# Kernel optimization log

Hardware: AMD Instinct MI355X
Metric: run time of the kernel (lower is better)

Reference implementation:

```python
import jax, jax.numpy as jnp
import numpy as np

B, H, W_DIM, C = 16, 128, 128, 256

def setup_inputs() -> dict:
    key = jax.random.key(0)
    k1, k2, k3 = jax.random.split(key, 3)
    grid = jax.random.normal(k1, (B, H, W_DIM, C), dtype=jnp.float32)
    # nn.Linear(2C, C): weight [C, 2C], bias [C]; store transposed for x @ W
    W = jax.random.normal(k2, (2 * C, C), dtype=jnp.float32) * (1.0 / np.sqrt(2 * C))
    b = jax.random.normal(k3, (C,), dtype=jnp.float32) * 0.01
    return {"grid": grid, "W": W, "b": b}

def reference(grid, W, b):
    # cumulative max along width (axis=2) and height (axis=1)
    x_cummax = jax.lax.cummax(grid, axis=2)
    y_cummax = jax.lax.cummax(grid, axis=1)
    result = jnp.concatenate([x_cummax, y_cummax], axis=-1)  # [B,H,W,2C]
    return result @ W + b  # [B,H,W,C]
```

## Files before the change

### kernel.cpp

```cpp
#include <hip/hip_runtime.h>
#include <hip/hip_fp16.h>

#define BB 16
#define HH 128
#define WW 128
#define CC 256

typedef __attribute__((ext_vector_type(8))) short s16x8;
typedef __attribute__((ext_vector_type(8))) unsigned short u16x8;
typedef __attribute__((ext_vector_type(4))) float f32x4;
typedef __attribute__((ext_vector_type(4))) int i32x4;

__device__ static inline unsigned short f2bf(float x) {
    union { float f; unsigned u; } v; v.f = x;
    unsigned r = v.u + 0x7fffu + ((v.u >> 16) & 1u);
    return (unsigned short)(r >> 16);
}
__device__ static inline float bf2f(unsigned short u) {
    union { unsigned u; float f; } v; v.u = (unsigned)u << 16; return v.f;
}
__device__ static inline unsigned short h2u(__half h) {
    unsigned short u; __builtin_memcpy(&u, &h, 2); return u;
}
__device__ static inline float u2f16(unsigned short u) {
    __half h; __builtin_memcpy(&h, &u, 2); return __half2float(h);
}
__device__ static inline int sidx(int row, int col) {
    return row * 256 + (((col >> 3) ^ (row & 7)) << 3) + (col & 7);
}
__device__ static inline int sidx4(int row, int c4) {
    return row * 256 + (((c4 >> 1) ^ (row & 7)) << 3) + (c4 & 1) * 4;
}

__global__ __launch_bounds__(256) void conv_w_kernel(const float* __restrict__ Wf,
                                                     unsigned short* __restrict__ Wt) {
    const int i = blockIdx.x * 256 + threadIdx.x;
    const int n = i & 255, k = i >> 8;
    const int hy = k >> 8, g = (k >> 3) & 31, j = k & 7;
    Wt[hy * 65536 + ((size_t)(g * 256 + n) << 3) + j] = f2bf(Wf[i]);
}

template <bool NT>
__device__ __forceinline__ void scan16_to_lds(const f32x4* __restrict__ base, size_t st,
                                              unsigned short* __restrict__ As,
                                              unsigned short* __restrict__ smax,
                                              int c4, int s) {
    const int row0 = s * 16;
    f32x4 buf[8], nxt[8];
    #pragma unroll
    for (int j = 0; j < 8; ++j)
        buf[j] = NT ? __builtin_nontemporal_load(base + (size_t)j * st)
                    : base[(size_t)j * st];
    __builtin_amdgcn_sched_group_barrier(0x20, 8, 0);
    #pragma unroll
    for (int j = 0; j < 8; ++j)
        nxt[j] = NT ? __builtin_nontemporal_load(base + (size_t)(8 + j) * st)
                    : base[(size_t)(8 + j) * st];
    __builtin_amdgcn_sched_group_barrier(0x20, 8, 0);
    f32x4 run = {-3.4e38f, -3.4e38f, -3.4e38f, -3.4e38f};
    #pragma unroll
    for (int j = 0; j < 8; ++j) {
        run[0] = fmaxf(run[0], buf[j][0]); run[1] = fmaxf(run[1], buf[j][1]);
        run[2] = fmaxf(run[2], buf[j][2]); run[3] = fmaxf(run[3], buf[j][3]);
        ushort4 o; o.x = f2bf(run[0]); o.y = f2bf(run[1]); o.z = f2bf(run[2]); o.w = f2bf(run[3]);
        *(ushort4*)(As + sidx4(row0 + j, c4)) = o;
    }
    #pragma unroll
    for (int j = 0; j < 8; ++j) {
        run[0] = fmaxf(run[0], nxt[j][0]); run[1] = fmaxf(run[1], nxt[j][1]);
        run[2] = fmaxf(run[2], nxt[j][2]); run[3] = fmaxf(run[3], nxt[j][3]);
        ushort4 o; o.x = f2bf(run[0]); o.y = f2bf(run[1]); o.z = f2bf(run[2]); o.w = f2bf(run[3]);
        *(ushort4*)(As + sidx4(row0 + 8 + j, c4)) = o;
    }
    ushort4 sm; sm.x = f2bf(run[0]); sm.y = f2bf(run[1]); sm.z = f2bf(run[2]); sm.w = f2bf(run[3]);
    *(ushort4*)(smax + s * 256 + c4 * 4) = sm;
}

__device__ __forceinline__ void carry_apply(unsigned short* __restrict__ As,
                                            const unsigned short* __restrict__ smax,
                                            int c4, int s) {
    if (s == 0) return;
    float4 cf = make_float4(-3.4e38f, -3.4e38f, -3.4e38f, -3.4e38f);
    for (int k = 0; k < s; ++k) {
        const ushort4 m = *(const ushort4*)(smax + k * 256 + c4 * 4);
        cf.x = fmaxf(cf.x, bf2f(m.x)); cf.y = fmaxf(cf.y, bf2f(m.y));
        cf.z = fmaxf(cf.z, bf2f(m.z)); cf.w = fmaxf(cf.w, bf2f(m.w));
    }
    ushort4 cb; cb.x = f2bf(cf.x); cb.y = f2bf(cf.y); cb.z = f2bf(cf.z); cb.w = f2bf(cf.w);
    const int row0 = s * 16;
    #pragma unroll
    for (int r = 0; r < 16; ++r) {
        unsigned short* pp = As + sidx4(row0 + r, c4);
        ushort4 v = *(ushort4*)(pp);
        ushort4 o;
        o.x = (bf2f(v.x) >= cf.x) ? v.x : cb.x;
        o.y = (bf2f(v.y) >= cf.y) ? v.y : cb.y;
        o.z = (bf2f(v.z) >= cf.z) ? v.z : cb.z;
        o.w = (bf2f(v.w) >= cf.w) ? v.w : cb.w;
        *(ushort4*)(pp) = o;
    }
}

template <bool ADD_BIAS>
__device__ __forceinline__ void gemm_stage(unsigned short* __restrict__ As,
                                           const s16x8* __restrict__ Wv,
                                           const float* __restrict__ bias, int t) {
    const int lane = t & 63, wid = t >> 6;
    const int wr = wid >> 2, wn = wid & 3;
    float bb[4];
    if (ADD_BIAS) {
        #pragma unroll
        for (int fn = 0; fn < 4; ++fn)
            bb[fn] = bias[wn * 64 + fn * 16 + (lane & 15)];
    }
    f32x4 acc[4][4];
    #pragma unroll
    for (int i = 0; i < 4; ++i)
        #pragma unroll
        for (int j = 0; j < 4; ++j) acc[i][j] = (f32x4){0.f, 0.f, 0.f, 0.f};

    #pragma unroll
    for (int q = 0; q < 8; ++q) {
        const int g = q * 4 + (lane >> 4);
        s16x8 af[4], bf[4];
        #pragma unroll
        for (int fm = 0; fm < 4; ++fm) {
            const int row = wr * 64 + fm * 16 + (lane & 15);
            af[fm] = *(const s16x8*)(As + row * 256 + ((g ^ (row & 7)) << 3));
        }
        #pragma unroll
        for (int fn = 0; fn < 4; ++fn)
            bf[fn] = Wv[g * 256 + wn * 64 + fn * 16 + (lane & 15)];
        #pragma unroll
        for (int fm = 0; fm < 4; ++fm)
            #pragma unroll
            for (int fn = 0; fn < 4; ++fn)
                acc[fm][fn] = __builtin_amdgcn_mfma_f32_16x16x32_bf16(
                    af[fm], bf[fn], acc[fm][fn], 0, 0, 0);
    }
    __syncthreads();
    #pragma unroll
    for (int fn = 0; fn < 4; ++fn) {
        const int col = wn * 64 + fn * 16 + (lane & 15);
        #pragma unroll
        for (int fm = 0; fm < 4; ++fm) {
            const int rbase = wr * 64 + fm * 16 + ((lane >> 4) << 2);
            #pragma unroll
            for (int r = 0; r < 4; ++r) {
                const float v = ADD_BIAS ? acc[fm][fn][r] + bb[fn] : acc[fm][fn][r];
                As[sidx(rbase + r, col)] = h2u(__float2half(v));
            }
        }
    }
    __syncthreads();
}

__global__ __launch_bounds__(512, 4) void hscan_gemm_kernel(const float* __restrict__ grid,
                                                            const float* __restrict__ bias,
                                                            const unsigned short* __restrict__ Wt,
                                                            unsigned short* __restrict__ partial) {
    __shared__ unsigned short As[32768];
    __shared__ unsigned short smax[2048];
    const int t = threadIdx.x;
    const int c4 = t & 63, s = t >> 6;
    const int b = blockIdx.x >> 7;
    const int w = blockIdx.x & 127;

    const f32x4* base = (const f32x4*)(grid + ((size_t)(b * 128 + s * 16) * 128 + w) * 256) + c4;
    scan16_to_lds<true>(base, 8192, As, smax, c4, s);
    __syncthreads();
    carry_apply(As, smax, c4, s);
    __syncthreads();

    gemm_stage<true>(As, (const s16x8*)(Wt + 65536), bias, t);

    #pragma unroll
    for (int it = 0; it < 8; ++it) {
        const int f = it * 4096 + t * 8;
        const int row = f >> 8, col = f & 255;
        const i32x4 v = *(const i32x4*)(As + sidx(row, col));
        *(i32x4*)(partial + (((size_t)b * 128 + row) * 128 + w) * 256 + col) = v;
    }
}

__global__ __launch_bounds__(512, 4) void wscan_gemm_kernel(const float* __restrict__ grid,
                                                            const unsigned short* __restrict__ Wt,
                                                            const unsigned short* __restrict__ partial,
                                                            float* __restrict__ out) {
    __shared__ unsigned short As[32768];
    __shared__ unsigned short smax[2048];
    const int t = threadIdx.x;
    const int c4 = t & 63, s = t >> 6;
    const size_t bh = blockIdx.x;

    const f32x4* base = (const f32x4*)(grid + (bh * 128 + (size_t)(s * 16)) * 256) + c4;
    scan16_to_lds<true>(base, 64, As, smax, c4, s);
    __syncthreads();
    carry_apply(As, smax, c4, s);
    __syncthreads();

    gemm_stage<false>(As, (const s16x8*)Wt, nullptr, t);

    #pragma unroll
    for (int it = 0; it < 8; ++it) {
        const int f = it * 4096 + t * 8;
        const int row = f >> 8, col = f & 255;
        const u16x8 lv = *(const u16x8*)(As + sidx(row, col));
        const size_t gi = bh * 32768 + (size_t)f;
        const u16x8 pv = __builtin_nontemporal_load((const u16x8*)(partial + gi));
        f32x4 o0, o1;
        #pragma unroll
        for (int k = 0; k < 4; ++k)
            o0[k] = u2f16((unsigned short)lv[k]) + u2f16((unsigned short)pv[k]);
        #pragma unroll
        for (int k = 0; k < 4; ++k)
            o1[k] = u2f16((unsigned short)lv[4 + k]) + u2f16((unsigned short)pv[4 + k]);
        __builtin_nontemporal_store(o0, (f32x4*)(out + gi));
        __builtin_nontemporal_store(o1, (f32x4*)(out + gi + 4));
    }
}

extern "C" void kernel_launch(void* const* d_in, const int* in_sizes, int n_in,
                              void* d_out, int out_size, void* d_ws, size_t ws_size,
                              hipStream_t stream) {
    const float* grid = (const float*)d_in[0];
    const float* Wf   = (const float*)d_in[1];
    const float* bias = (const float*)d_in[2];
    float* out        = (float*)d_out;

    unsigned short* partial = (unsigned short*)d_ws;
    unsigned short* Wt      = (unsigned short*)((char*)d_ws + (size_t)134217728);

    conv_w_kernel<<<512, 256, 0, stream>>>(Wf, Wt);
    hscan_gemm_kernel<<<2048, 512, 0, stream>>>(grid, bias, Wt, partial);
    wscan_gemm_kernel<<<2048, 512, 0, stream>>>(grid, Wt, partial, out);
}
```

Measured before the change: 238.4 us.

## Split scan+GEMM into two 64-row halves, prefetching second half during first GEMM

```diff
diff --git a/kernel.cpp b/kernel.cpp
--- a/kernel.cpp
+++ b/kernel.cpp
@@ -41,22 +41,20 @@
 }
 
 template <bool NT>
-__device__ __forceinline__ void scan16_to_lds(const f32x4* __restrict__ base, size_t st,
-                                              unsigned short* __restrict__ As,
-                                              unsigned short* __restrict__ smax,
-                                              int c4, int s) {
-    const int row0 = s * 16;
-    f32x4 buf[8], nxt[8];
+__device__ __forceinline__ void load8(const f32x4* __restrict__ base, size_t st,
+                                      f32x4 buf[8]) {
     #pragma unroll
     for (int j = 0; j < 8; ++j)
         buf[j] = NT ? __builtin_nontemporal_load(base + (size_t)j * st)
                     : base[(size_t)j * st];
     __builtin_amdgcn_sched_group_barrier(0x20, 8, 0);
-    #pragma unroll
-    for (int j = 0; j < 8; ++j)
-        nxt[j] = NT ? __builtin_nontemporal_load(base + (size_t)(8 + j) * st)
-                    : base[(size_t)(8 + j) * st];
-    __builtin_amdgcn_sched_group_barrier(0x20, 8, 0);
+}
+
+__device__ __forceinline__ void consume8(const f32x4 buf[8],
+                                         unsigned short* __restrict__ As,
+                                         unsigned short* __restrict__ smax,
+                                         int c4, int s, int par) {
+    const int row0 = s * 8;
     f32x4 run = {-3.4e38f, -3.4e38f, -3.4e38f, -3.4e38f};
     #pragma unroll
     for (int j = 0; j < 8; ++j) {
@@ -65,74 +63,76 @@
         ushort4 o; o.x = f2bf(run[0]); o.y = f2bf(run[1]); o.z = f2bf(run[2]); o.w = f2bf(run[3]);
         *(ushort4*)(As + sidx4(row0 + j, c4)) = o;
     }
-    #pragma unroll
-    for (int j = 0; j < 8; ++j) {
-        run[0] = fmaxf(run[0], nxt[j][0]); run[1] = fmaxf(run[1], nxt[j][1]);
-        run[2] = fmaxf(run[2], nxt[j][2]); run[3] = fmaxf(run[3], nxt[j][3]);
-        ushort4 o; o.x = f2bf(run[0]); o.y = f2bf(run[1]); o.z = f2bf(run[2]); o.w = f2bf(run[3]);
-        *(ushort4*)(As + sidx4(row0 + 8 + j, c4)) = o;
-    }
     ushort4 sm; sm.x = f2bf(run[0]); sm.y = f2bf(run[1]); sm.z = f2bf(run[2]); sm.w = f2bf(run[3]);
-    *(ushort4*)(smax + s * 256 + c4 * 4) = sm;
-}
-
-__device__ __forceinline__ void carry_apply(unsigned short* __restrict__ As,
-                                            const unsigned short* __restrict__ smax,
-                                            int c4, int s) {
-    if (s == 0) return;
+    *(ushort4*)(smax + par * 2048 + s * 256 + c4 * 4) = sm;
+}
+
+__device__ __forceinline__ void carry8(unsigned short* __restrict__ As,
+                                       const unsigned short* __restrict__ smax,
+                                       int c4, int s, int par, bool cross) {
     float4 cf = make_float4(-3.4e38f, -3.4e38f, -3.4e38f, -3.4e38f);
+    if (cross) {
+        #pragma unroll
+        for (int k = 0; k < 8; ++k) {
+            const ushort4 m = *(const ushort4*)(smax + (par ^ 1) * 2048 + k * 256 + c4 * 4);
+            cf.x = fmaxf(cf.x, bf2f(m.x)); cf.y = fmaxf(cf.y, bf2f(m.y));
+            cf.z = fmaxf(cf.z, bf2f(m.z)); cf.w = fmaxf(cf.w, bf2f(m.w));
+        }
+    }
     for (int k = 0; k < s; ++k) {
-        const ushort4 m = *(const ushort4*)(smax + k * 256 + c4 * 4);
+        const ushort4 m = *(const ushort4*)(smax + par * 2048 + k * 256 + c4 * 4);
         cf.x = fmaxf(cf.x, bf2f(m.x)); cf.y = fmaxf(cf.y, bf2f(m.y));
         cf.z = fmaxf(cf.z, bf2f(m.z)); cf.w = fmaxf(cf.w, bf2f(m.w));
     }
-    ushort4 cb; cb.x = f2bf(cf.x); cb.y = f2bf(cf.y); cb.z = f2bf(cf.z); cb.w = f2bf(cf.w);
-    const int row0 = s * 16;
-    #pragma unroll
-    for (int r = 0; r < 16; ++r) {
-        unsigned short* pp = As + sidx4(row0 + r, c4);
-        ushort4 v = *(ushort4*)(pp);
-        ushort4 o;
-        o.x = (bf2f(v.x) >= cf.x) ? v.x : cb.x;
-        o.y = (bf2f(v.y) >= cf.y) ? v.y : cb.y;
-        o.z = (bf2f(v.z) >= cf.z) ? v.z : cb.z;
-        o.w = (bf2f(v.w) >= cf.w) ? v.w : cb.w;
-        *(ushort4*)(pp) = o;
+    if (cross || s) {
+        ushort4 cb; cb.x = f2bf(cf.x); cb.y = f2bf(cf.y); cb.z = f2bf(cf.z); cb.w = f2bf(cf.w);
+        const int row0 = s * 8;
+        #pragma unroll
+        for (int r = 0; r < 8; ++r) {
+            unsigned short* pp = As + sidx4(row0 + r, c4);
+            ushort4 v = *(ushort4*)pp;
+            ushort4 o;
+            o.x = (bf2f(v.x) >= cf.x) ? v.x : cb.x;
+            o.y = (bf2f(v.y) >= cf.y) ? v.y : cb.y;
+            o.z = (bf2f(v.z) >= cf.z) ? v.z : cb.z;
+            o.w = (bf2f(v.w) >= cf.w) ? v.w : cb.w;
+            *(ushort4*)pp = o;
+        }
     }
 }
 
 template <bool ADD_BIAS>
-__device__ __forceinline__ void gemm_stage(unsigned short* __restrict__ As,
-                                           const s16x8* __restrict__ Wv,
-                                           const float* __restrict__ bias, int t) {
+__device__ __forceinline__ void gemm_stage64(unsigned short* __restrict__ As,
+                                             const s16x8* __restrict__ Wv,
+                                             const float* __restrict__ bias, int t) {
     const int lane = t & 63, wid = t >> 6;
-    const int wr = wid >> 2, wn = wid & 3;
+    const int wm = wid >> 2, wn = wid & 3;
     float bb[4];
     if (ADD_BIAS) {
         #pragma unroll
         for (int fn = 0; fn < 4; ++fn)
             bb[fn] = bias[wn * 64 + fn * 16 + (lane & 15)];
     }
-    f32x4 acc[4][4];
-    #pragma unroll
-    for (int i = 0; i < 4; ++i)
+    f32x4 acc[2][4];
+    #pragma unroll
+    for (int i = 0; i < 2; ++i)
         #pragma unroll
         for (int j = 0; j < 4; ++j) acc[i][j] = (f32x4){0.f, 0.f, 0.f, 0.f};
 
     #pragma unroll
     for (int q = 0; q < 8; ++q) {
         const int g = q * 4 + (lane >> 4);
-        s16x8 af[4], bf[4];
-        #pragma unroll
-        for (int fm = 0; fm < 4; ++fm) {
-            const int row = wr * 64 + fm * 16 + (lane & 15);
+        s16x8 af[2], bf[4];
+        #pragma unroll
+        for (int fm = 0; fm < 2; ++fm) {
+            const int row = wm * 32 + fm * 16 + (lane & 15);
             af[fm] = *(const s16x8*)(As + row * 256 + ((g ^ (row & 7)) << 3));
         }
         #pragma unroll
         for (int fn = 0; fn < 4; ++fn)
             bf[fn] = Wv[g * 256 + wn * 64 + fn * 16 + (lane & 15)];
         #pragma unroll
-        for (int fm = 0; fm < 4; ++fm)
+        for (int fm = 0; fm < 2; ++fm)
             #pragma unroll
             for (int fn = 0; fn < 4; ++fn)
                 acc[fm][fn] = __builtin_amdgcn_mfma_f32_16x16x32_bf16(
@@ -143,8 +143,8 @@
     for (int fn = 0; fn < 4; ++fn) {
         const int col = wn * 64 + fn * 16 + (lane & 15);
         #pragma unroll
-        for (int fm = 0; fm < 4; ++fm) {
-            const int rbase = wr * 64 + fm * 16 + ((lane >> 4) << 2);
+        for (int fm = 0; fm < 2; ++fm) {
+            const int rbase = wm * 32 + fm * 16 + ((lane >> 4) << 2);
             #pragma unroll
             for (int r = 0; r < 4; ++r) {
                 const float v = ADD_BIAS ? acc[fm][fn][r] + bb[fn] : acc[fm][fn][r];
@@ -159,27 +159,49 @@
                                                             const float* __restrict__ bias,
                                                             const unsigned short* __restrict__ Wt,
                                                             unsigned short* __restrict__ partial) {
-    __shared__ unsigned short As[32768];
-    __shared__ unsigned short smax[2048];
+    __shared__ unsigned short lds[36864];
+    unsigned short* A  = lds;
+    unsigned short* Bv = lds + 16384;
+    unsigned short* sx = lds + 32768;
     const int t = threadIdx.x;
     const int c4 = t & 63, s = t >> 6;
     const int b = blockIdx.x >> 7;
     const int w = blockIdx.x & 127;
-
-    const f32x4* base = (const f32x4*)(grid + ((size_t)(b * 128 + s * 16) * 128 + w) * 256) + c4;
-    scan16_to_lds<true>(base, 8192, As, smax, c4, s);
-    __syncthreads();
-    carry_apply(As, smax, c4, s);
-    __syncthreads();
-
-    gemm_stage<true>(As, (const s16x8*)(Wt + 65536), bias, t);
-
-    #pragma unroll
-    for (int it = 0; it < 8; ++it) {
-        const int f = it * 4096 + t * 8;
-        const int row = f >> 8, col = f & 255;
-        const i32x4 v = *(const i32x4*)(As + sidx(row, col));
+    const s16x8* Wy = (const s16x8*)(Wt + 65536);
+
+    const f32x4* g0 = (const f32x4*)grid + ((size_t)(b * 128 + s * 8) * 128 + w) * 64 + c4;
+    f32x4 buf[8];
+    load8<false>(g0, 8192, buf);
+    consume8(buf, A, sx, c4, s, 0);
+    __syncthreads();
+    carry8(A, sx, c4, s, 0, false);
+    __syncthreads();
+
+    load8<false>(g0 + (size_t)64 * 8192, 8192, buf);
+
+    gemm_stage64<true>(A, Wy, bias, t);
+
+    #pragma unroll
+    for (int it = 0; it < 4; ++it) {
+        const int f = it * 4096 + t * 8;
+        const int row = f >> 8, col = f & 255;
+        const i32x4 v = *(const i32x4*)(A + sidx(row, col));
         *(i32x4*)(partial + (((size_t)b * 128 + row) * 128 + w) * 256 + col) = v;
+    }
+
+    consume8(buf, Bv, sx, c4, s, 1);
+    __syncthreads();
+    carry8(Bv, sx, c4, s, 1, true);
+    __syncthreads();
+
+    gemm_stage64<true>(Bv, Wy, bias, t);
+
+    #pragma unroll
+    for (int it = 0; it < 4; ++it) {
+        const int f = it * 4096 + t * 8;
+        const int row = f >> 8, col = f & 255;
+        const i32x4 v = *(const i32x4*)(Bv + sidx(row, col));
+        *(i32x4*)(partial + (((size_t)b * 128 + 64 + row) * 128 + w) * 256 + col) = v;
     }
 }
 
@@ -187,26 +209,58 @@
                                                             const unsigned short* __restrict__ Wt,
                                                             const unsigned short* __restrict__ partial,
                                                             float* __restrict__ out) {
-    __shared__ unsigned short As[32768];
-    __shared__ unsigned short smax[2048];
+    __shared__ unsigned short lds[36864];
+    unsigned short* A  = lds;
+    unsigned short* Bv = lds + 16384;
+    unsigned short* sx = lds + 32768;
     const int t = threadIdx.x;
     const int c4 = t & 63, s = t >> 6;
     const size_t bh = blockIdx.x;
-
-    const f32x4* base = (const f32x4*)(grid + (bh * 128 + (size_t)(s * 16)) * 256) + c4;
-    scan16_to_lds<true>(base, 64, As, smax, c4, s);
-    __syncthreads();
-    carry_apply(As, smax, c4, s);
-    __syncthreads();
-
-    gemm_stage<false>(As, (const s16x8*)Wt, nullptr, t);
-
-    #pragma unroll
-    for (int it = 0; it < 8; ++it) {
-        const int f = it * 4096 + t * 8;
-        const int row = f >> 8, col = f & 255;
-        const u16x8 lv = *(const u16x8*)(As + sidx(row, col));
+    const s16x8* Wx = (const s16x8*)Wt;
+
+    const f32x4* g0 = (const f32x4*)grid + (bh * 128 + (size_t)(s * 8)) * 64 + c4;
+    f32x4 buf[8];
+    load8<true>(g0, 64, buf);
+    consume8(buf, A, sx, c4, s, 0);
+    __syncthreads();
+    carry8(A, sx, c4, s, 0, false);
+    __syncthreads();
+
+    load8<true>(g0 + (size_t)64 * 64, 64, buf);
+
+    gemm_stage64<false>(A, Wx, nullptr, t);
+
+    #pragma unroll
+    for (int it = 0; it < 4; ++it) {
+        const int f = it * 4096 + t * 8;
+        const int row = f >> 8, col = f & 255;
+        const u16x8 lv = *(const u16x8*)(A + sidx(row, col));
         const size_t gi = bh * 32768 + (size_t)f;
+        const u16x8 pv = __builtin_nontemporal_load((const u16x8*)(partial + gi));
+        f32x4 o0, o1;
+        #pragma unroll
+        for (int k = 0; k < 4; ++k)
+            o0[k] = u2f16((unsigned short)lv[k]) + u2f16((unsigned short)pv[k]);
+        #pragma unroll
+        for (int k = 0; k < 4; ++k)
+            o1[k] = u2f16((unsigned short)lv[4 + k]) + u2f16((unsigned short)pv[4 + k]);
+        __builtin_nontemporal_store(o0, (f32x4*)(out + gi));
+        __builtin_nontemporal_store(o1, (f32x4*)(out + gi + 4));
+    }
+
+    consume8(buf, Bv, sx, c4, s, 1);
+    __syncthreads();
+    carry8(Bv, sx, c4, s, 1, true);
+    __syncthreads();
+
+    gemm_stage64<false>(Bv, Wx, nullptr, t);
+
+    #pragma unroll
+    for (int it = 0; it < 4; ++it) {
+        const int f = it * 4096 + t * 8;
+        const int row = f >> 8, col = f & 255;
+        const u16x8 lv = *(const u16x8*)(Bv + sidx(row, col));
+        const size_t gi = bh * 32768 + 16384 + (size_t)f;
         const u16x8 pv = __builtin_nontemporal_load((const u16x8*)(partial + gi));
         f32x4 o0, o1;
         #pragma unroll
```

Measured after the change: 250.2 us. +4.9%, slower.
